# Performance work log

Measured on AMD Instinct MI355X. Metric: run time of the kernel, lower is better.

Reference implementation:

```python
import jax, jax.numpy as jnp
import numpy as np
from jax import lax

B, C, H, W = 4, 128, 256, 256
HEADS = 8
HIDDEN = int(C * 2)  # ffn_expansion_factor=2
THETA = 0.7


def _p(key, shape, scale=0.05):
    return jax.random.normal(key, shape, dtype=jnp.float32) * scale


def setup_inputs() -> dict:
    key = jax.random.key(0)
    ks = jax.random.split(key, 32)
    inp = {
        'ms': jax.random.normal(ks[0], (B, C, H, W), dtype=jnp.float32),
        'pan': jax.random.normal(ks[1], (B, C, H, W), dtype=jnp.float32),
        # LayerNorms (WithBias)
        'ln1_w': jnp.ones((C,), jnp.float32),
        'ln1_b': jnp.zeros((C,), jnp.float32),
        'ln2_w': jnp.ones((2 * C,), jnp.float32),
        'ln2_b': jnp.zeros((2 * C,), jnp.float32),
        # Attention (bias=False)
        'qkv_w': _p(ks[2], (C, C)),            # 1x1 conv weight [out,in]
        'dw_w': _p(ks[3], (C, 1, 3, 3)),       # depthwise 3x3 (Conv2d_cd)
        'temperature': jnp.ones((HEADS, 1, 1), jnp.float32),
        'proj_w': _p(ks[4], (C, C)),
        # Freprocess (default bias=True)
        'pre1_w': _p(ks[5], (C, C)), 'pre1_b': jnp.zeros((C,), jnp.float32),
        'pre2_w': _p(ks[6], (C, C)), 'pre2_b': jnp.zeros((C,), jnp.float32),
        'amp1_w': _p(ks[7], (C, 2 * C)), 'amp1_b': jnp.zeros((C,), jnp.float32),
        'amp2_w': _p(ks[8], (C, C)), 'amp2_b': jnp.zeros((C,), jnp.float32),
        'pha1_w': _p(ks[9], (C, 2 * C)), 'pha1_b': jnp.zeros((C,), jnp.float32),
        'pha2_w': _p(ks[10], (C, C)), 'pha2_b': jnp.zeros((C,), jnp.float32),
        'post_w': _p(ks[11], (C, C)), 'post_b': jnp.zeros((C,), jnp.float32),
        # FFN (bias=False)
        'pin_w': _p(ks[12], (2 * HIDDEN, 2 * C)),
        'pout_w': _p(ks[13], (C, HIDDEN)),
    }
    return inp


def conv1x1(x, w, b=None):
    y = jnp.einsum('bchw,oc->bohw', x, w)
    if b is not None:
        y = y + b[None, :, None, None]
    return y


def layernorm_c(x, w, b):
    # per-pixel LayerNorm over channel dim (torch var unbiased=False, eps=1e-5)
    mu = jnp.mean(x, axis=1, keepdims=True)
    var = jnp.mean((x - mu) ** 2, axis=1, keepdims=True)
    return (x - mu) / jnp.sqrt(var + 1e-5) * w[None, :, None, None] + b[None, :, None, None]


def dwconv_cd(x, w):
    # central-difference depthwise conv: dw3x3(x) - theta * (sum(kernel) * x)
    y = lax.conv_general_dilated(x, w, (1, 1), ((1, 1), (1, 1)),
                                 dimension_numbers=('NCHW', 'OIHW', 'NCHW'),
                                 feature_group_count=x.shape[1])
    ksum = w.sum(axis=(1, 2, 3))  # (C,)
    return y - THETA * x * ksum[None, :, None, None]


def attention(nms, npan, qkv_w, dw_w, temperature, proj_w):
    b, c, h, w = nms.shape
    ch = c // HEADS
    q = dwconv_cd(conv1x1(nms, qkv_w), dw_w)
    kv = dwconv_cd(conv1x1(npan, qkv_w), dw_w)  # k == v in source
    q = q.reshape(b, HEADS, ch, h * w)
    k = kv.reshape(b, HEADS, ch, h * w)
    v = k
    q = q / jnp.maximum(jnp.linalg.norm(q, axis=-1, keepdims=True), 1e-12)
    k = k / jnp.maximum(jnp.linalg.norm(k, axis=-1, keepdims=True), 1e-12)
    attn = jnp.einsum('bhcn,bhdn->bhcd', q, k) * temperature[None]
    attn = jax.nn.softmax(attn, axis=-1)
    out = jnp.einsum('bhcd,bhdn->bhcn', attn, v).reshape(b, c, h, w)
    return conv1x1(out, proj_w)


def freprocess(msf, panf, pre1_w, pre1_b, pre2_w, pre2_b,
               amp1_w, amp1_b, amp2_w, amp2_b,
               pha1_w, pha1_b, pha2_w, pha2_b, post_w, post_b):
    h, w = msf.shape[-2:]
    msF = jnp.fft.rfft2(conv1x1(msf, pre1_w, pre1_b) + 1e-8)
    panF = jnp.fft.rfft2(conv1x1(panf, pre2_w, pre2_b) + 1e-8)
    amp_in = jnp.concatenate([jnp.abs(msF), jnp.abs(panF)], axis=1)
    pha_in = jnp.concatenate([jnp.angle(msF), jnp.angle(panF)], axis=1)
    amp = conv1x1(jax.nn.leaky_relu(conv1x1(amp_in, amp1_w, amp1_b), 0.1), amp2_w, amp2_b)
    pha = conv1x1(jax.nn.leaky_relu(conv1x1(pha_in, pha1_w, pha1_b), 0.1), pha2_w, pha2_b)
    real = amp * jnp.cos(pha) + 1e-8
    imag = amp * jnp.sin(pha) + 1e-8
    out = jax.lax.complex(real, imag) + 1e-8
    out = jnp.abs(jnp.fft.irfft2(out, s=(h, w)))
    return conv1x1(out, post_w, post_b)


def ffn(x, pin_w, pout_w):
    y = conv1x1(x, pin_w)
    x1, x2 = jnp.split(y, 2, axis=1)
    return conv1x1(jax.nn.gelu(x1, approximate=False) * x2, pout_w)


def reference(ms, pan, ln1_w, ln1_b, ln2_w, ln2_b, qkv_w, dw_w, temperature,
              proj_w, pre1_w, pre1_b, pre2_w, pre2_b, amp1_w, amp1_b, amp2_w,
              amp2_b, pha1_w, pha1_b, pha2_w, pha2_b, post_w, post_b,
              pin_w, pout_w):
    x = ms + attention(layernorm_c(ms, ln1_w, ln1_b),
                       layernorm_c(pan, ln1_w, ln1_b),
                       qkv_w, dw_w, temperature, proj_w)
    frefuse = freprocess(ms, pan, pre1_w, pre1_b, pre2_w, pre2_b,
                         amp1_w, amp1_b, amp2_w, amp2_b,
                         pha1_w, pha1_b, pha2_w, pha2_b, post_w, post_b)
    frespa = jnp.concatenate([x, frefuse], axis=1)
    x = x + ffn(layernorm_c(frespa, ln2_w, ln2_b), pin_w, pout_w)
    return x
```

## Files before the change

### kernel.cpp

```cpp
#include <hip/hip_runtime.h>
#include <math.h>

#define B_ 4
#define C_ 128
#define HW_ 65536
#define H__ 256
#define KF_ 129
#define PLANEF_ 33024

typedef __attribute__((ext_vector_type(8))) short short8v;
typedef __attribute__((ext_vector_type(4))) float f32x4;
typedef __attribute__((ext_vector_type(4))) unsigned short ush4;
typedef __attribute__((ext_vector_type(8))) unsigned short ush8;

__device__ __forceinline__ unsigned short f2bf(float f) {
    union { float f; unsigned u; } v; v.f = f;
    return (unsigned short)((v.u + 0x7FFFu + ((v.u >> 16) & 1u)) >> 16);
}
__device__ __forceinline__ float bf2f(unsigned short s) {
    union { unsigned u; float f; } v; v.u = (unsigned)s << 16;
    return v.f;
}
__device__ __forceinline__ unsigned pack2bf(float2 v) {
    return (unsigned)f2bf(v.x) | ((unsigned)f2bf(v.y) << 16);
}
__device__ __forceinline__ float2 upk(unsigned u) {
    return make_float2(bf2f((unsigned short)(u & 0xffff)), bf2f((unsigned short)(u >> 16)));
}
__device__ __forceinline__ float geluf(float x) {
    float z = 0.70710678118654752f * fabsf(x);
    float t = __fdividef(1.f, fmaf(0.3275911f, z, 1.f));
    float p = fmaf(1.061405429f, t, -1.453152027f);
    p = fmaf(p, t, 1.421413741f);
    p = fmaf(p, t, -0.284496736f);
    p = fmaf(p, t, 0.254829592f);
    p = p * t;
    float erfv = 1.f - p * __expf(-z * z);
    float cdf = (x >= 0.f) ? fmaf(0.5f, erfv, 0.5f) : fmaf(-0.5f, erfv, 0.5f);
    return x * cdf;
}
__device__ __forceinline__ float fatan2(float y, float x) {
    float ax = fabsf(x), ay = fabsf(y);
    float mx = fmaxf(ax, ay), mn = fminf(ax, ay);
    float a = __fdividef(mn, fmaxf(mx, 1e-38f));
    float s = a * a;
    float r = fmaf(0.0208351f, s, -0.0851330f);
    r = fmaf(r, s, 0.1801410f);
    r = fmaf(r, s, -0.3302995f);
    r = fmaf(r, s, 0.9998660f);
    r = r * a;
    if (ay > ax) r = 1.57079632679489662f - r;
    if (x < 0.f) r = 3.14159265358979324f - r;
    return copysignf(r, y);
}
template<int W>
__device__ __forceinline__ char* swz_ptr(unsigned short (*xs)[W], int px, int cb) {
    return (char*)xs + px * (W * 2) + (cb ^ (((px >> 2) & 7) << 4));
}

__global__ __launch_bounds__(256) void tobf16_kernel(const float* __restrict__ src,
                                                     unsigned short* __restrict__ dst, int n)
{
    int i = blockIdx.x * 256 + threadIdx.x;
    if (i < n) dst[i] = f2bf(src[i]);
}

__global__ __launch_bounds__(128) void foldln_kernel(const float* __restrict__ W,
                                                     const float* __restrict__ lnw,
                                                     const float* __restrict__ lnb,
                                                     unsigned short* __restrict__ Wb,
                                                     float* __restrict__ wsum, float* __restrict__ bsum,
                                                     int Cc)
{
    int o = blockIdx.x, t = threadIdx.x;
    float sw = 0.f, sb = 0.f;
    for (int c = t; c < Cc; c += 128) {
        float w = W[(size_t)o * Cc + c];
        float fw = w * lnw[c];
        unsigned short us = f2bf(fw);
        Wb[(size_t)o * Cc + c] = us;
        sw += bf2f(us);
        sb += w * lnb[c];
    }
    __shared__ float r1[128], r2[128];
    r1[t] = sw; r2[t] = sb; __syncthreads();
    for (int st = 64; st; st >>= 1) {
        if (t < st) { r1[t] += r1[t + st]; r2[t] += r2[t + st]; }
        __syncthreads();
    }
    if (!t) { wsum[o] = r1[0]; bsum[o] = r2[0]; }
}

__global__ __launch_bounds__(256) void poutperm_kernel(const float* __restrict__ src,
                                                       unsigned short* __restrict__ dst)
{
    int i = blockIdx.x * 256 + threadIdx.x;
    int half = i >> 14, rem = i & 16383, o = rem >> 7, kp = rem & 127;
    int h = (kp >> 5) * 64 + half * 32 + (kp & 31);
    dst[i] = f2bf(src[o * 256 + h]);
}

__global__ void pinc_kernel(const float* __restrict__ bb, const float* __restrict__ ws,
                            float4* __restrict__ pinC)
{
    int i = threadIdx.x;
    if (i < 256) pinC[i] = make_float4(bb[i], ws[i], bb[i + 256], ws[i + 256]);
}

__global__ void ksum_kernel(const float* __restrict__ dw, float* __restrict__ ks)
{
    int c = threadIdx.x;
    if (c < C_) {
        float s = 0.f;
        for (int k = 0; k < 9; ++k) s += dw[c * 9 + k];
        ks[c] = s;
    }
}

__global__ __launch_bounds__(256) void zero2_kernel(float* __restrict__ a, float* __restrict__ b, int n)
{
    int i = blockIdx.x * 256 + threadIdx.x;
    if (i < n) { a[i] = 0.f; b[i] = 0.f; }
}

template<int INBF, int OUTBF, int PRO, bool LNF>
__global__ __launch_bounds__(256, 3) void mconv2(
    const void* __restrict__ Xv, size_t sx,
    const unsigned short* __restrict__ Wb, int wstride,
    const float* __restrict__ bias,
    const float* __restrict__ res, size_t sres,
    void* __restrict__ Yv, size_t sy, int plane, int flags,
    const float* __restrict__ wsum, const float* __restrict__ bsum)
{
    __shared__ unsigned short xs[128][136];
    __shared__ float2 lnred[LNF ? 8 : 1][LNF ? 128 : 1];
    __shared__ float2 lnmi[LNF ? 128 : 1];
    const int t = threadIdx.x;
    const int bz = blockIdx.z;
    const int p0 = blockIdx.x * 128;
    const int lane = t & 63;
    const int wr = t >> 7, wc = (t >> 6) & 1;
    const int lr = lane >> 4, lc = lane & 15;

    if constexpr (INBF == 0) {
        const float* Xb = (const float*)Xv + (size_t)bz * sx;
        const int px4 = t & 31;
        float s0 = 0.f, s1 = 0.f, s2v = 0.f, s3 = 0.f;
        float q0 = 0.f, q1 = 0.f, q2 = 0.f, q3 = 0.f;
#pragma unroll
        for (int g = 0; g < 2; ++g) {
            float4 st[8];
#pragma unroll
            for (int i = 0; i < 8; ++i) {
                int e = t + (g * 8 + i) * 256;
                int c = e >> 5;
                st[i] = *(const float4*)(Xb + (size_t)c * plane + p0 + px4 * 4);
            }
#pragma unroll
            for (int i = 0; i < 8; ++i) {
                int e = t + (g * 8 + i) * 256;
                int c = e >> 5;
                float a0 = st[i].x, a1 = st[i].y, a2 = st[i].z, a3 = st[i].w;
                if constexpr (PRO == 1) {
                    a0 = a0 > 0.f ? a0 : 0.1f * a0;
                    a1 = a1 > 0.f ? a1 : 0.1f * a1;
                    a2 = a2 > 0.f ? a2 : 0.1f * a2;
                    a3 = a3 > 0.f ? a3 : 0.1f * a3;
                }
                if constexpr (LNF) {
                    s0 += a0; q0 += a0 * a0;
                    s1 += a1; q1 += a1 * a1;
                    s2v += a2; q2 += a2 * a2;
                    s3 += a3; q3 += a3 * a3;
                }
                *(unsigned short*)swz_ptr(xs, px4 * 4 + 0, 2 * c) = f2bf(a0);
                *(unsigned short*)swz_ptr(xs, px4 * 4 + 1, 2 * c) = f2bf(a1);
                *(unsigned short*)swz_ptr(xs, px4 * 4 + 2, 2 * c) = f2bf(a2);
                *(unsigned short*)swz_ptr(xs, px4 * 4 + 3, 2 * c) = f2bf(a3);
            }
        }
        if constexpr (LNF) {
            lnred[t >> 5][px4 * 4 + 0] = make_float2(s0, q0);
            lnred[t >> 5][px4 * 4 + 1] = make_float2(s1, q1);
            lnred[t >> 5][px4 * 4 + 2] = make_float2(s2v, q2);
            lnred[t >> 5][px4 * 4 + 3] = make_float2(s3, q3);
        }
    } else {
        const unsigned short* Xb = (const unsigned short*)Xv + (size_t)bz * sx;
        ush8 st[8];
#pragma unroll
        for (int i = 0; i < 8; ++i) {
            int e = t + i * 256;
            int c = e >> 4, px8 = e & 15;
            st[i] = *(const ush8*)(Xb + (size_t)c * plane + p0 + px8 * 8);
        }
#pragma unroll
        for (int i = 0; i < 8; ++i) {
            int e = t + i * 256;
            int c = e >> 4, px8 = e & 15;
#pragma unroll
            for (int j = 0; j < 8; ++j) {
                unsigned short us = (unsigned short)st[i][j];
                if constexpr (PRO == 1) {
                    float f = bf2f(us);
                    f = f > 0.f ? f : 0.1f * f;
                    us = f2bf(f);
                }
                *(unsigned short*)swz_ptr(xs, px8 * 8 + j, 2 * c) = us;
            }
        }
    }
    __syncthreads();
    if constexpr (LNF) {
        if (t < 128) {
            float ss = 0.f, qq = 0.f;
#pragma unroll
            for (int j = 0; j < 8; ++j) { float2 a = lnred[j][t]; ss += a.x; qq += a.y; }
            float m = ss * (1.f / 128.f);
            float inv = rsqrtf(qq * (1.f / 128.f) - m * m + 1e-5f);
            lnmi[t] = make_float2(m, inv);
        }
        __syncthreads();
    }

    f32x4 acc[4][4];
#pragma unroll
    for (int mi = 0; mi < 4; ++mi)
#pragma unroll
        for (int ni = 0; ni < 4; ++ni) acc[mi][ni] = (f32x4){0.f, 0.f, 0.f, 0.f};

#pragma unroll
    for (int kk = 0; kk < 128; kk += 32) {
        short8v bfr[4];
#pragma unroll
        for (int ni = 0; ni < 4; ++ni)
            bfr[ni] = *(const short8v*)swz_ptr(xs, wc * 64 + ni * 16 + lc, 2 * (kk + lr * 8));
#pragma unroll
        for (int mi = 0; mi < 4; ++mi) {
            int row = wr * 64 + mi * 16 + lc;
            short8v afr = *(const short8v*)(Wb + (size_t)row * wstride + kk + lr * 8);
#pragma unroll
            for (int ni = 0; ni < 4; ++ni)
                acc[mi][ni] = __builtin_amdgcn_mfma_f32_16x16x32_bf16(afr, bfr[ni], acc[mi][ni], 0, 0, 0);
        }
    }

    float2 mrow[4];
    if constexpr (LNF) {
#pragma unroll
        for (int ni = 0; ni < 4; ++ni) mrow[ni] = lnmi[wc * 64 + ni * 16 + lc];
    }

#pragma unroll
    for (int mi = 0; mi < 4; ++mi) {
        int ob = wr * 64 + mi * 16 + lr * 4;
#pragma unroll
        for (int r = 0; r < 4; ++r) {
            int o = ob + r;
            float bv = 0.f, wso = 0.f;
            if constexpr (LNF) { bv = bsum[o]; wso = wsum[o]; }
            else { if (bias) bv = bias[o]; if (flags & 1) bv += 1e-8f; }
#pragma unroll
            for (int ni = 0; ni < 4; ++ni) {
                int px = wc * 64 + ni * 16 + lc;
                float v;
                if constexpr (LNF) {
                    float m = mrow[ni].x, inv = mrow[ni].y;
                    v = acc[mi][ni][r] * inv + bv - m * inv * wso;
                } else {
                    v = acc[mi][ni][r] + bv;
                }
                if constexpr (OUTBF == 0) {
                    float* Y = (float*)Yv;
                    size_t yi = (size_t)bz * sy + (size_t)o * plane + p0 + px;
                    if (res) v += res[(size_t)bz * sres + (size_t)o * plane + p0 + px];
                    Y[yi] = v;
                } else {
                    unsigned short* Y = (unsigned short*)Yv;
                    Y[(size_t)bz * sy + (size_t)o * plane + p0 + px] = f2bf(v);
                }
            }
        }
    }
}

__global__ __launch_bounds__(256, 2) void apconv2(
    const unsigned* __restrict__ T1, const unsigned* __restrict__ T2, size_t sT,
    const unsigned short* __restrict__ Wa1, const unsigned short* __restrict__ Wp1,
    const unsigned short* __restrict__ Wa2, const unsigned short* __restrict__ Wp2,
    const float* __restrict__ ba1, const float* __restrict__ bp1,
    const float* __restrict__ ba2, const float* __restrict__ bp2,
    unsigned short* __restrict__ AMP, unsigned short* __restrict__ PHA, size_t sO)
{
    __shared__ __align__(16) unsigned short buf[2][128][72];
    const int t = threadIdx.x;
    const int bz = blockIdx.z;
    const int p0 = blockIdx.x * 128;
    const int lane = t & 63;
    const int wr = t >> 7, wc = (t >> 6) & 1;
    const int lr = lane >> 4, lc = lane & 15;
    const int px2 = t & 63;

    typedef unsigned short (*row72)[72];
    typedef unsigned short (*row144)[144];
    row72 xa = (row72)buf[0];
    row72 xp = (row72)buf[1];
    row144 hb = (row144)&buf[0][0][0];

    f32x4 aa[4][4], ap[4][4];
#pragma unroll
    for (int mi = 0; mi < 4; ++mi)
#pragma unroll
        for (int ni = 0; ni < 4; ++ni) { aa[mi][ni] = (f32x4){0.f,0.f,0.f,0.f}; ap[mi][ni] = (f32x4){0.f,0.f,0.f,0.f}; }

    for (int ch = 0; ch < 256; ch += 64) {
        const unsigned* Ts = ((ch < 128) ? T1 : T2) + (size_t)bz * sT + (size_t)(ch & 127) * PLANEF_;
#pragma unroll
        for (int g = 0; g < 2; ++g) {
            uint2 st[8];
#pragma unroll
            for (int i = 0; i < 8; ++i) {
                int e = t + (g * 8 + i) * 256;
                int c = e >> 6;
                st[i] = *(const uint2*)(Ts + (size_t)c * PLANEF_ + p0 + px2 * 2);
            }
#pragma unroll
            for (int i = 0; i < 8; ++i) {
                int e = t + (g * 8 + i) * 256;
                int c = e >> 6;
                float2 z0 = upk(st[i].x), z1 = upk(st[i].y);
                float m0 = sqrtf(z0.x * z0.x + z0.y * z0.y);
                float m1 = sqrtf(z1.x * z1.x + z1.y * z1.y);
                float a0 = fatan2(z0.y, z0.x);
                float a1 = fatan2(z1.y, z1.x);
                *(unsigned short*)swz_ptr(xa, px2 * 2 + 0, 2 * c) = f2bf(m0);
                *(unsigned short*)swz_ptr(xa, px2 * 2 + 1, 2 * c) = f2bf(m1);
                *(unsigned short*)swz_ptr(xp, px2 * 2 + 0, 2 * c) = f2bf(a0);
                *(unsigned short*)swz_ptr(xp, px2 * 2 + 1, 2 * c) = f2bf(a1);
            }
        }
        __syncthreads();
#pragma unroll
        for (int kk = 0; kk < 64; kk += 32) {
            short8v bfa[4], bfp[4];
#pragma unroll
            for (int ni = 0; ni < 4; ++ni) {
                bfa[ni] = *(const short8v*)swz_ptr(xa, wc * 64 + ni * 16 + lc, 2 * (kk + lr * 8));
                bfp[ni] = *(const short8v*)swz_ptr(xp, wc * 64 + ni * 16 + lc, 2 * (kk + lr * 8));
            }
#pragma unroll
            for (int mi = 0; mi < 4; ++mi) {
                int row = wr * 64 + mi * 16 + lc;
                short8v afa = *(const short8v*)(Wa1 + (size_t)row * 256 + ch + kk + lr * 8);
                short8v afp = *(const short8v*)(Wp1 + (size_t)row * 256 + ch + kk + lr * 8);
#pragma unroll
                for (int ni = 0; ni < 4; ++ni) {
                    aa[mi][ni] = __builtin_amdgcn_mfma_f32_16x16x32_bf16(afa, bfa[ni], aa[mi][ni], 0, 0, 0);
                    ap[mi][ni] = __builtin_amdgcn_mfma_f32_16x16x32_bf16(afp, bfp[ni], ap[mi][ni], 0, 0, 0);
                }
            }
        }
        __syncthreads();
    }

#pragma unroll
    for (int mi = 0; mi < 4; ++mi)
#pragma unroll
        for (int r = 0; r < 4; ++r) {
            int o = wr * 64 + mi * 16 + lr * 4 + r;
            float bva = ba1[o];
#pragma unroll
            for (int ni = 0; ni < 4; ++ni) {
                int px = wc * 64 + ni * 16 + lc;
                float v = aa[mi][ni][r] + bva;
                v = v > 0.f ? v : 0.1f * v;
                *(unsigned short*)swz_ptr(hb, px, 2 * o) = f2bf(v);
            }
        }
    __syncthreads();
    {
        f32x4 acc[4][4];
#pragma unroll
        for (int mi = 0; mi < 4; ++mi)
#pragma unroll
            for (int ni = 0; ni < 4; ++ni) acc[mi][ni] = (f32x4){0.f,0.f,0.f,0.f};
#pragma unroll
        for (int kk = 0; kk < 128; kk += 32) {
            short8v bfr[4];
#pragma unroll
            for (int ni = 0; ni < 4; ++ni)
                bfr[ni] = *(const short8v*)swz_ptr(hb, wc * 64 + ni * 16 + lc, 2 * (kk + lr * 8));
#pragma unroll
            for (int mi = 0; mi < 4; ++mi) {
                int row = wr * 64 + mi * 16 + lc;
                short8v afr = *(const short8v*)(Wa2 + (size_t)row * 128 + kk + lr * 8);
#pragma unroll
                for (int ni = 0; ni < 4; ++ni)
                    acc[mi][ni] = __builtin_amdgcn_mfma_f32_16x16x32_bf16(afr, bfr[ni], acc[mi][ni], 0, 0, 0);
            }
        }
#pragma unroll
        for (int mi = 0; mi < 4; ++mi)
#pragma unroll
            for (int r = 0; r < 4; ++r) {
                int o = wr * 64 + mi * 16 + lr * 4 + r;
                float bv = ba2[o];
#pragma unroll
                for (int ni = 0; ni < 4; ++ni) {
                    int px = wc * 64 + ni * 16 + lc;
                    AMP[(size_t)bz * sO + (size_t)o * PLANEF_ + p0 + px] = f2bf(acc[mi][ni][r] + bv);
                }
            }
    }
    __syncthreads();

#pragma unroll
    for (int mi = 0; mi < 4; ++mi)
#pragma unroll
        for (int r = 0; r < 4; ++r) {
            int o = wr * 64 + mi * 16 + lr * 4 + r;
            float bvp = bp1[o];
#pragma unroll
            for (int ni = 0; ni < 4; ++ni) {
                int px = wc * 64 + ni * 16 + lc;
                float v = ap[mi][ni][r] + bvp;
                v = v > 0.f ? v : 0.1f * v;
                *(unsigned short*)swz_ptr(hb, px, 2 * o) = f2bf(v);
            }
        }
    __syncthreads();
    {
        f32x4 acc[4][4];
#pragma unroll
        for (int mi = 0; mi < 4; ++mi)
#pragma unroll
            for (int ni = 0; ni < 4; ++ni) acc[mi][ni] = (f32x4){0.f,0.f,0.f,0.f};
#pragma unroll
        for (int kk = 0; kk < 128; kk += 32) {
            short8v bfr[4];
#pragma unroll
            for (int ni = 0; ni < 4; ++ni)
                bfr[ni] = *(const short8v*)swz_ptr(hb, wc * 64 + ni * 16 + lc, 2 * (kk + lr * 8));
#pragma unroll
            for (int mi = 0; mi < 4; ++mi) {
                int row = wr * 64 + mi * 16 + lc;
                short8v afr = *(const short8v*)(Wp2 + (size_t)row * 128 + kk + lr * 8);
#pragma unroll
                for (int ni = 0; ni < 4; ++ni)
                    acc[mi][ni] = __builtin_amdgcn_mfma_f32_16x16x32_bf16(afr, bfr[ni], acc[mi][ni], 0, 0, 0);
            }
        }
#pragma unroll
        for (int mi = 0; mi < 4; ++mi)
#pragma unroll
            for (int r = 0; r < 4; ++r) {
                int o = wr * 64 + mi * 16 + lr * 4 + r;
                float bv = bp2[o];
#pragma unroll
                for (int ni = 0; ni < 4; ++ni) {
                    int px = wc * 64 + ni * 16 + lc;
                    PHA[(size_t)bz * sO + (size_t)o * PLANEF_ + p0 + px] = f2bf(acc[mi][ni][r] + bv);
                }
            }
    }
}

__global__ __launch_bounds__(256, 3) void ffn_mfma5(
    const float* __restrict__ x, const unsigned short* __restrict__ fre,
    const unsigned short* __restrict__ pinb,
    const unsigned short* __restrict__ pout2,
    const float4* __restrict__ pinC,
    float* __restrict__ out)
{
    __shared__ unsigned short xs[64][264];
    __shared__ unsigned short hs[64][136];
    __shared__ float2 muinv[64];
    float2* sred = (float2*)&hs[0][0];
    const int b = blockIdx.y;
    const size_t p0 = (size_t)blockIdx.x * 64;
    const int t = threadIdx.x;
    const int wave = t >> 6, lane = t & 63;
    const int lr = lane >> 4, lc = lane & 15;
    const int px4 = t & 15;

    float s0 = 0.f, s1 = 0.f, s2v = 0.f, s3 = 0.f;
    float q0 = 0.f, q1 = 0.f, q2 = 0.f, q3 = 0.f;
    {
        float4 stx[8];
        ush4 stf[8];
#pragma unroll
        for (int i = 0; i < 8; ++i) {
            int e = t + i * 256;
            int c = e >> 4;
            stx[i] = *(const float4*)(x + ((size_t)b * 128 + c) * HW_ + p0 + px4 * 4);
        }
#pragma unroll
        for (int i = 0; i < 8; ++i) {
            int e = t + i * 256;
            int c = e >> 4;
            stf[i] = *(const ush4*)(fre + (size_t)b * 8388608 + (size_t)c * HW_ + p0 + px4 * 4);
        }
#pragma unroll
        for (int i = 0; i < 8; ++i) {
            int e = t + i * 256;
            int c = e >> 4;
            float a0 = stx[i].x, a1 = stx[i].y, a2 = stx[i].z, a3 = stx[i].w;
            s0 += a0; q0 += a0 * a0;
            s1 += a1; q1 += a1 * a1;
            s2v += a2; q2 += a2 * a2;
            s3 += a3; q3 += a3 * a3;
            *(unsigned short*)swz_ptr(xs, px4 * 4 + 0, 2 * c) = f2bf(a0);
            *(unsigned short*)swz_ptr(xs, px4 * 4 + 1, 2 * c) = f2bf(a1);
            *(unsigned short*)swz_ptr(xs, px4 * 4 + 2, 2 * c) = f2bf(a2);
            *(unsigned short*)swz_ptr(xs, px4 * 4 + 3, 2 * c) = f2bf(a3);
        }
#pragma unroll
        for (int i = 0; i < 8; ++i) {
            int e = t + i * 256;
            int c = e >> 4;
            float a0 = bf2f((unsigned short)stf[i][0]);
            float a1 = bf2f((unsigned short)stf[i][1]);
            float a2 = bf2f((unsigned short)stf[i][2]);
            float a3 = bf2f((unsigned short)stf[i][3]);
            s0 += a0; q0 += a0 * a0;
            s1 += a1; q1 += a1 * a1;
            s2v += a2; q2 += a2 * a2;
            s3 += a3; q3 += a3 * a3;
            *(unsigned short*)swz_ptr(xs, px4 * 4 + 0, 2 * (128 + c)) = (unsigned short)stf[i][0];
            *(unsigned short*)swz_ptr(xs, px4 * 4 + 1, 2 * (128 + c)) = (unsigned short)stf[i][1];
            *(unsigned short*)swz_ptr(xs, px4 * 4 + 2, 2 * (128 + c)) = (unsigned short)stf[i][2];
            *(unsigned short*)swz_ptr(xs, px4 * 4 + 3, 2 * (128 + c)) = (unsigned short)stf[i][3];
        }
    }
    sred[(t >> 4) * 64 + px4 * 4 + 0] = make_float2(s0, q0);
    sred[(t >> 4) * 64 + px4 * 4 + 1] = make_float2(s1, q1);
    sred[(t >> 4) * 64 + px4 * 4 + 2] = make_float2(s2v, q2);
    sred[(t >> 4) * 64 + px4 * 4 + 3] = make_float2(s3, q3);
    __syncthreads();
    if (t < 64) {
        float ss = 0.f, qq = 0.f;
#pragma unroll
        for (int j = 0; j < 16; ++j) { float2 a = sred[j * 64 + t]; ss += a.x; qq += a.y; }
        float m = ss * (1.f / 256.f);
        float inv = rsqrtf(qq * (1.f / 256.f) - m * m + 1e-5f);
        muinv[t] = make_float2(m, inv);
    }
    __syncthreads();

    float2 mrow[4];
#pragma unroll
    for (int ni = 0; ni < 4; ++ni) mrow[ni] = muinv[ni * 16 + lc];

    f32x4 oc[2][4];
#pragma unroll
    for (int mi = 0; mi < 2; ++mi)
#pragma unroll
        for (int ni = 0; ni < 4; ++ni) oc[mi][ni] = (f32x4){0.f, 0.f, 0.f, 0.f};

#pragma unroll
    for (int half = 0; half < 2; ++half) {
        f32x4 a1[2][4], a2[2][4];
#pragma unroll
        for (int mi = 0; mi < 2; ++mi)
#pragma unroll
            for (int ni = 0; ni < 4; ++ni) { a1[mi][ni] = (f32x4){0.f,0.f,0.f,0.f}; a2[mi][ni] = (f32x4){0.f,0.f,0.f,0.f}; }

#pragma unroll
        for (int k0 = 0; k0 < 256; k0 += 32) {
            short8v bfr[4];
#pragma unroll
            for (int ni = 0; ni < 4; ++ni)
                bfr[ni] = *(const short8v*)swz_ptr(xs, ni * 16 + lc, 2 * (k0 + lr * 8));
#pragma unroll
            for (int mi = 0; mi < 2; ++mi) {
                int hrow = wave * 64 + half * 32 + mi * 16 + lc;
                short8v af1 = *(const short8v*)(pinb + (size_t)hrow * 256 + k0 + lr * 8);
                short8v af2 = *(const short8v*)(pinb + (size_t)(hrow + 256) * 256 + k0 + lr * 8);
#pragma unroll
                for (int ni = 0; ni < 4; ++ni) {
                    a1[mi][ni] = __builtin_amdgcn_mfma_f32_16x16x32_bf16(af1, bfr[ni], a1[mi][ni], 0, 0, 0);
                    a2[mi][ni] = __builtin_amdgcn_mfma_f32_16x16x32_bf16(af2, bfr[ni], a2[mi][ni], 0, 0, 0);
                }
            }
        }
        __syncthreads();
#pragma unroll
        for (int mi = 0; mi < 2; ++mi)
#pragma unroll
            for (int r = 0; r < 4; ++r) {
                int ho = wave * 64 + half * 32 + mi * 16 + lr * 4 + r;
                float4 bwc = pinC[ho];
                int kp = wave * 32 + mi * 16 + lr * 4 + r;
#pragma unroll
                for (int ni = 0; ni < 4; ++ni) {
                    float m = mrow[ni].x, inv = mrow[ni].y;
                    float v1 = a1[mi][ni][r] * inv + bwc.x - m * inv * bwc.y;
                    float v2 = a2[mi][ni][r] * inv + bwc.z - m * inv * bwc.w;
                    hs[ni * 16 + lc][kp] = f2bf(geluf(v1) * v2);
                }
            }
        __syncthreads();
#pragma unroll
        for (int k0 = 0; k0 < 128; k0 += 32) {
            short8v bfr2[4];
#pragma unroll
            for (int ni = 0; ni < 4; ++ni)
                bfr2[ni] = *(const short8v*)&hs[ni * 16 + lc][k0 + lr * 8];
#pragma unroll
            for (int mi = 0; mi < 2; ++mi) {
                int orow = wave * 32 + mi * 16 + lc;
                short8v af = *(const short8v*)(pout2 + half * 16384 + orow * 128 + k0 + lr * 8);
#pragma unroll
                for (int ni = 0; ni < 4; ++ni)
                    oc[mi][ni] = __builtin_amdgcn_mfma_f32_16x16x32_bf16(af, bfr2[ni], oc[mi][ni], 0, 0, 0);
            }
        }
    }

#pragma unroll
    for (int mi = 0; mi < 2; ++mi)
#pragma unroll
        for (int r = 0; r < 4; ++r) {
            int o = wave * 32 + mi * 16 + lr * 4 + r;
#pragma unroll
            for (int ni = 0; ni < 4; ++ni) {
                size_t yi = ((size_t)b * 128 + o) * HW_ + p0 + ni * 16 + lc;
                out[yi] = oc[mi][ni][r] + x[yi];
            }
        }
}

__global__ __launch_bounds__(256) void dwconv2(const unsigned short* __restrict__ X, size_t sx,
                                               const float* __restrict__ w9,
                                               const float* __restrict__ ksum,
                                               unsigned short* __restrict__ Y, size_t sy,
                                               float* __restrict__ ssq)
{
    int bz = blockIdx.z;
    int c = blockIdx.y;
    int p4 = blockIdx.x * 256 + threadIdx.x;
    int p0 = p4 * 4;
    int i = p0 >> 8, j0 = p0 & 255;
    const unsigned short* xp = X + (size_t)bz * sx + (size_t)c * HW_;
    const float* wc = w9 + c * 9;
    float a[4] = {0.f, 0.f, 0.f, 0.f};
    float ctr[4];
#pragma unroll
    for (int di = -1; di <= 1; ++di) {
        int ii = i + di;
        if (ii < 0 || ii > 255) continue;
        const unsigned short* row = xp + ii * 256;
        ush4 m4 = *(const ush4*)(row + j0);
        float lft = (j0 > 0) ? bf2f(row[j0 - 1]) : 0.f;
        float rgt = (j0 < 252) ? bf2f(row[j0 + 4]) : 0.f;
        float v[6] = {lft, bf2f((unsigned short)m4[0]), bf2f((unsigned short)m4[1]),
                      bf2f((unsigned short)m4[2]), bf2f((unsigned short)m4[3]), rgt};
        if (di == 0) { ctr[0] = v[1]; ctr[1] = v[2]; ctr[2] = v[3]; ctr[3] = v[4]; }
        float w0 = wc[(di + 1) * 3], w1 = wc[(di + 1) * 3 + 1], w2 = wc[(di + 1) * 3 + 2];
#pragma unroll
        for (int k = 0; k < 4; ++k) a[k] += w0 * v[k] + w1 * v[k + 1] + w2 * v[k + 2];
    }
    float km = 0.7f * ksum[c];
    float o0 = a[0] - km * ctr[0], o1 = a[1] - km * ctr[1];
    float o2 = a[2] - km * ctr[2], o3 = a[3] - km * ctr[3];
    ush4 ov;
    ov[0] = f2bf(o0); ov[1] = f2bf(o1); ov[2] = f2bf(o2); ov[3] = f2bf(o3);
    *(ush4*)(Y + (size_t)bz * sy + (size_t)c * HW_ + p0) = ov;

    float q = o0 * o0 + o1 * o1 + o2 * o2 + o3 * o3;
    __shared__ float red[256];
    red[threadIdx.x] = q; __syncthreads();
    for (int st = 128; st; st >>= 1) {
        if (threadIdx.x < st) red[threadIdx.x] += red[threadIdx.x + st];
        __syncthreads();
    }
    if (!threadIdx.x) atomicAdd(&ssq[bz * C_ + c], red[0]);
}

__global__ __launch_bounds__(256) void gram_kernel(const unsigned short* __restrict__ Q, size_t sq,
                                                   const unsigned short* __restrict__ K, size_t sk,
                                                   float* __restrict__ part)
{
    int sl = blockIdx.x, h = blockIdx.y, bz = blockIdx.z;
    const unsigned short* qb = Q + (size_t)bz * sq + (size_t)(h * 16) * HW_;
    const unsigned short* kb = K + (size_t)bz * sk + (size_t)(h * 16) * HW_;
    __shared__ __align__(16) float qs[16][68];
    __shared__ __align__(16) float ks[16][68];
    int c = threadIdx.x >> 4, d = threadIdx.x & 15;
    float acc = 0.f;
    for (int n0 = sl * 2048; n0 < (sl + 1) * 2048; n0 += 64) {
        {
            int cc = threadIdx.x >> 4, nn4 = threadIdx.x & 15;
            ush4 qv = *(const ush4*)(qb + (size_t)cc * HW_ + n0 + nn4 * 4);
            ush4 kv = *(const ush4*)(kb + (size_t)cc * HW_ + n0 + nn4 * 4);
#pragma unroll
            for (int j = 0; j < 4; ++j) {
                qs[cc][nn4 * 4 + j] = bf2f((unsigned short)qv[j]);
                ks[cc][nn4 * 4 + j] = bf2f((unsigned short)kv[j]);
            }
        }
        __syncthreads();
#pragma unroll
        for (int nn = 0; nn < 64; nn += 4) {
            float4 qv = *(const float4*)&qs[c][nn];
            float4 kv = *(const float4*)&ks[d][nn];
            acc += qv.x * kv.x + qv.y * kv.y + qv.z * kv.z + qv.w * kv.w;
        }
        __syncthreads();
    }
    part[((size_t)(bz * 8 + h) * 32 + sl) * 256 + threadIdx.x] = acc;
}

__global__ __launch_bounds__(256) void softmax_kernel(const float* __restrict__ part,
                                                      const float* __restrict__ nqsq,
                                                      const float* __restrict__ nksq,
                                                      const float* __restrict__ temp,
                                                      float* __restrict__ attn)
{
    int h = blockIdx.x, bz = blockIdx.y;
    int t = threadIdx.x;
    int c = t >> 4, d = t & 15;
    float g = 0.f;
    for (int sl = 0; sl < 32; ++sl) g += part[((size_t)(bz * 8 + h) * 32 + sl) * 256 + t];
    float nqv = fmaxf(sqrtf(nqsq[bz * C_ + h * 16 + c]), 1e-12f);
    float nkv = fmaxf(sqrtf(nksq[bz * C_ + h * 16 + d]), 1e-12f);
    g *= temp[h] / (nqv * nkv);
    float m = g;
#pragma unroll
    for (int off = 8; off; off >>= 1) m = fmaxf(m, __shfl_xor(m, off, 16));
    float e = __expf(g - m);
    float ssum = e;
#pragma unroll
    for (int off = 8; off; off >>= 1) ssum += __shfl_xor(ssum, off, 16);
    attn[(bz * 8 + h) * 256 + t] = e / ssum;
}

__global__ __launch_bounds__(256) void av_kernel(const float* __restrict__ attn,
                                                 const unsigned short* __restrict__ V, size_t sv,
                                                 unsigned short* __restrict__ Y, size_t sy)
{
    __shared__ __align__(16) float kv[16][260];
    __shared__ __align__(16) float at[16][16];
    int tile = blockIdx.x, h = blockIdx.y, bz = blockIdx.z;
    int n0 = tile * 256, t = threadIdx.x;
    const unsigned short* vb = V + (size_t)bz * sv + (size_t)(h * 16) * HW_;
    at[t >> 4][t & 15] = attn[(size_t)(bz * 8 + h) * 256 + (t & 15) * 16 + (t >> 4)];
#pragma unroll
    for (int i = 0; i < 4; ++i) {
        int e = t + i * 256;
        int d = e >> 6, nn4 = e & 63;
        ush4 v4 = *(const ush4*)(vb + (size_t)d * HW_ + n0 + nn4 * 4);
#pragma unroll
        for (int j = 0; j < 4; ++j) kv[d][nn4 * 4 + j] = bf2f((unsigned short)v4[j]);
    }
    __syncthreads();
    float acc[16];
#pragma unroll
    for (int cc = 0; cc < 16; ++cc) acc[cc] = 0.f;
#pragma unroll
    for (int d = 0; d < 16; ++d) {
        float kvv = kv[d][t];
        float4 a0 = *(const float4*)&at[d][0];
        float4 a1 = *(const float4*)&at[d][4];
        float4 a2 = *(const float4*)&at[d][8];
        float4 a3 = *(const float4*)&at[d][12];
        acc[0]  += a0.x * kvv; acc[1]  += a0.y * kvv; acc[2]  += a0.z * kvv; acc[3]  += a0.w * kvv;
        acc[4]  += a1.x * kvv; acc[5]  += a1.y * kvv; acc[6]  += a1.z * kvv; acc[7]  += a1.w * kvv;
        acc[8]  += a2.x * kvv; acc[9]  += a2.y * kvv; acc[10] += a2.z * kvv; acc[11] += a2.w * kvv;
        acc[12] += a3.x * kvv; acc[13] += a3.y * kvv; acc[14] += a3.z * kvv; acc[15] += a3.w * kvv;
    }
    unsigned short* yb = Y + (size_t)bz * sy + (size_t)(h * 16) * HW_ + n0 + t;
#pragma unroll
    for (int cc = 0; cc < 16; ++cc) yb[(size_t)cc * HW_] = f2bf(acc[cc]);
}

__device__ __forceinline__ void fft_stages(float2* row, const float2* tw, int lane)
{
#pragma unroll
    for (int s = 1; s <= 8; ++s) {
        const int half = 1 << (s - 1);
#pragma unroll
        for (int r = 0; r < 4; ++r) {
            int jb = lane + r * 32;
            int j = jb & (half - 1);
            int g = jb >> (s - 1);
            int i1 = (g << s) + j;
            float2 w = tw[j << (8 - s)];
            float2 u = row[i1];
            float2 q = row[i1 + half];
            float2 v = make_float2(q.x * w.x - q.y * w.y, q.x * w.y + q.y * w.x);
            row[i1]        = make_float2(u.x + v.x, u.y + v.y);
            row[i1 + half] = make_float2(u.x - v.x, u.y - v.y);
        }
        __builtin_amdgcn_wave_barrier();
    }
    __syncthreads();
}

#define PI2_ 6.28318530717958647692f

__global__ __launch_bounds__(256) void rfft_rowsT(const unsigned short* __restrict__ X, size_t sx,
                                                  unsigned* __restrict__ T, size_t st)
{
    __shared__ float2 sd[8][256];
    __shared__ float2 tw[128];
    int t = threadIdx.x;
    int bz = blockIdx.y;
    if (t < 128) { float sn, cs; __sincosf(-PI2_ * (float)t * (1.f / 256.f), &sn, &cs); tw[t] = make_float2(cs, sn); }
    size_t r0 = (size_t)blockIdx.x * 8;
    int c = (int)(r0 >> 8), h0 = (int)(r0 & 255);
    const unsigned short* Xb = X + (size_t)bz * sx;
#pragma unroll
    for (int ii = 0; ii < 2; ++ii) {
        int e = t + ii * 256;
        int j = e >> 6, i4 = e & 63;
        ush4 v4 = *(const ush4*)(Xb + (r0 + j) * 256 + i4 * 4);
#pragma unroll
        for (int k2 = 0; k2 < 4; ++k2)
            sd[j][__brev((unsigned)(i4 * 4 + k2)) >> 24] = make_float2(bf2f((unsigned short)v4[k2]), 0.f);
    }
    __syncthreads();
    fft_stages(sd[t >> 5], tw, t & 31);
    unsigned* base = T + (size_t)bz * st + (size_t)c * PLANEF_;
    for (int e = t; e < 8 * 129; e += 256) {
        int j = e & 7, k = e >> 3;
        base[(size_t)k * 256 + h0 + j] = pack2bf(sd[j][k]);
    }
}

__global__ __launch_bounds__(256) void cfftT_fwd(unsigned* __restrict__ T, size_t st)
{
    __shared__ float2 sd[8][256];
    __shared__ float2 tw[128];
    int t = threadIdx.x;
    int bz = blockIdx.z;
    if (t < 128) { float sn, cs; __sincosf(-PI2_ * (float)t * (1.f / 256.f), &sn, &cs); tw[t] = make_float2(cs, sn); }
    int k0 = blockIdx.x * 8;
    int c = blockIdx.y;
    unsigned* base = T + (size_t)bz * st + (size_t)c * PLANEF_;
    for (int e = t; e < 2048; e += 256) {
        int j = e >> 8, i = e & 255;
        int k = k0 + j;
        float2 v = (k < KF_) ? upk(base[(size_t)k * 256 + i]) : make_float2(0.f, 0.f);
        sd[j][__brev((unsigned)i) >> 24] = v;
    }
    __syncthreads();
    fft_stages(sd[t >> 5], tw, t & 31);
    for (int e = t; e < 2048; e += 256) {
        int j = e >> 8, i = e & 255;
        int k = k0 + j;
        if (k < KF_) base[(size_t)k * 256 + i] = pack2bf(sd[j][i]);
    }
}

__global__ __launch_bounds__(256) void cifft_combine(const unsigned short* __restrict__ amp, size_t sa,
                                                     const unsigned short* __restrict__ pha, size_t sp,
                                                     unsigned* __restrict__ S, size_t ss)
{
    __shared__ float2 sd[8][256];
    __shared__ float2 tw[128];
    int t = threadIdx.x;
    int bz = blockIdx.z;
    if (t < 128) { float sn, cs; __sincosf(PI2_ * (float)t * (1.f / 256.f), &sn, &cs); tw[t] = make_float2(cs, sn); }
    int k0 = blockIdx.x * 8;
    int c = blockIdx.y;
    const unsigned short* ab = amp + (size_t)bz * sa + (size_t)c * PLANEF_;
    const unsigned short* pb = pha + (size_t)bz * sp + (size_t)c * PLANEF_;
    for (int e = t; e < 2048; e += 256) {
        int j = e >> 8, i = e & 255;
        int k = k0 + j;
        float2 v = make_float2(0.f, 0.f);
        if (k < KF_) {
            float a = bf2f(ab[(size_t)k * 256 + i]);
            float p = bf2f(pb[(size_t)k * 256 + i]);
            float sn, cs;
            __sincosf(p, &sn, &cs);
            v = make_float2(a * cs + 2e-8f, a * sn + 1e-8f);
        }
        sd[j][__brev((unsigned)i) >> 24] = v;
    }
    __syncthreads();
    fft_stages(sd[t >> 5], tw, t & 31);
    unsigned* base = S + (size_t)bz * ss + (size_t)c * PLANEF_;
    for (int e = t; e < 2048; e += 256) {
        int j = e & 7, h = e >> 3;
        int k = k0 + j;
        if (k < KF_) {
            float2 o = sd[j][h];
            base[(size_t)h * KF_ + k] = pack2bf(make_float2(o.x * (1.f / 256.f), o.y * (1.f / 256.f)));
        }
    }
}

__global__ __launch_bounds__(256) void irfft_rows8_abs(const unsigned* __restrict__ S, size_t ss,
                                                       unsigned short* __restrict__ Y, size_t sy)
{
    __shared__ float2 sd[8][256];
    __shared__ float2 tw[128];
    int t = threadIdx.x;
    int bz = blockIdx.y;
    if (t < 128) { float sn, cs; __sincosf(PI2_ * (float)t * (1.f / 256.f), &sn, &cs); tw[t] = make_float2(cs, sn); }
    size_t r0 = (size_t)blockIdx.x * 8;
    const unsigned* Sb = S + (size_t)bz * ss;
    for (int e = t; e < 2048; e += 256) {
        int j = e >> 8, i = e & 255;
        const unsigned* row = Sb + (r0 + j) * 129;
        float2 v;
        if (i < 129) v = upk(row[i]);
        else { float2 w2 = upk(row[256 - i]); v = make_float2(w2.x, -w2.y); }
        sd[j][__brev((unsigned)i) >> 24] = v;
    }
    __syncthreads();
    fft_stages(sd[t >> 5], tw, t & 31);
    unsigned short* Yb = Y + (size_t)bz * sy;
    for (int e = t; e < 2048; e += 256) {
        int j = e >> 8, i = e & 255;
        Yb[(r0 + j) * 256 + i] = f2bf(fabsf(sd[j][i].x * (1.f / 256.f)));
    }
}

extern "C" void kernel_launch(void* const* d_in, const int* in_sizes, int n_in,
                              void* d_out, int out_size, void* d_ws, size_t ws_size,
                              hipStream_t stream)
{
    (void)in_sizes; (void)n_in; (void)out_size;
    const float* ms    = (const float*)d_in[0];
    const float* pan   = (const float*)d_in[1];
    const float* ln1w  = (const float*)d_in[2];
    const float* ln1b  = (const float*)d_in[3];
    const float* ln2w  = (const float*)d_in[4];
    const float* ln2b  = (const float*)d_in[5];
    const float* qkvw  = (const float*)d_in[6];
    const float* dww   = (const float*)d_in[7];
    const float* temp  = (const float*)d_in[8];
    const float* projw = (const float*)d_in[9];
    const float* pre1w = (const float*)d_in[10];
    const float* pre1b = (const float*)d_in[11];
    const float* pre2w = (const float*)d_in[12];
    const float* pre2b = (const float*)d_in[13];
    const float* amp1w = (const float*)d_in[14];
    const float* amp1b = (const float*)d_in[15];
    const float* amp2w = (const float*)d_in[16];
    const float* amp2b = (const float*)d_in[17];
    const float* pha1w = (const float*)d_in[18];
    const float* pha1b = (const float*)d_in[19];
    const float* pha2w = (const float*)d_in[20];
    const float* pha2b = (const float*)d_in[21];
    const float* postw = (const float*)d_in[22];
    const float* postb = (const float*)d_in[23];
    const float* pinw  = (const float*)d_in[24];
    const float* poutw = (const float*)d_in[25];

    const size_t SLOT  = 8454144;
    const size_t CHWu  = 8388608;
    const size_t CPFu  = 4227072;
    const size_t SPECu = 4227072;
    const size_t PARAMU = 344064;
    const size_t PARAMF = 273792;

    auto needB = [&](int nb) -> size_t {
        return 2ull * (33554432ull + (size_t)nb * 3ull * SLOT + PARAMU) + 4ull * PARAMF + 64;
    };
    int NB = (ws_size >= needB(4)) ? 4 : ((ws_size >= needB(2)) ? 2 : 1);

    unsigned short* F  = (unsigned short*)d_ws;
    unsigned short* U0 = F + 33554432;
    unsigned short* U1 = U0 + (size_t)NB * SLOT;
    unsigned short* U2 = U1 + (size_t)NB * SLOT;
    unsigned short* w_qkv   = U2 + (size_t)NB * SLOT;
    unsigned short* w_proj  = w_qkv  + 16384;
    unsigned short* w_pre1  = w_proj + 16384;
    unsigned short* w_pre2  = w_pre1 + 16384;
    unsigned short* w_post  = w_pre2 + 16384;
    unsigned short* w_amp1  = w_post + 16384;
    unsigned short* w_pha1  = w_amp1 + 32768;
    unsigned short* w_amp2  = w_pha1 + 32768;
    unsigned short* w_pha2  = w_amp2 + 16384;
    unsigned short* w_pin   = w_pha2 + 16384;
    unsigned short* w_pout2 = w_pin  + 131072;
    float* fpar   = (float*)(w_pout2 + 32768);
    float* ksumP  = fpar;
    float* nqsq   = ksumP + 128;
    float* nksq   = nqsq  + 512;
    float* attnP  = nksq  + 512;
    float* partP  = attnP + 8192;
    float* qkv_ws = partP + 262144;
    float* qkv_bb = qkv_ws + 128;
    float* pin_ws = qkv_bb + 128;
    float* pin_bb = pin_ws + 512;
    float* pinC   = pin_bb + 512;

    float* xout = (float*)d_out;

    auto CVT = [&](const float* src, unsigned short* dst, int n) {
        tobf16_kernel<<<(n + 255) / 256, 256, 0, stream>>>(src, dst, n);
    };
    foldln_kernel<<<128, 128, 0, stream>>>(qkvw, ln1w, ln1b, w_qkv, qkv_ws, qkv_bb, 128);
    foldln_kernel<<<512, 128, 0, stream>>>(pinw, ln2w, ln2b, w_pin, pin_ws, pin_bb, 256);
    CVT(projw, w_proj, 16384);
    CVT(pre1w, w_pre1, 16384); CVT(pre2w, w_pre2, 16384);
    CVT(postw, w_post, 16384);
    CVT(amp1w, w_amp1, 32768); CVT(pha1w, w_pha1, 32768);
    CVT(amp2w, w_amp2, 16384); CVT(pha2w, w_pha2, 16384);
    poutperm_kernel<<<128, 256, 0, stream>>>(poutw, w_pout2);
    pinc_kernel<<<1, 256, 0, stream>>>(pin_bb, pin_ws, (float4*)pinC);
    ksum_kernel<<<1, 128, 0, stream>>>(dww, ksumP);

    const size_t CHW = (size_t)C_ * HW_;
    const float* NUL = nullptr;

    for (int b0 = 0; b0 < B_; b0 += NB) {
        const float* msb  = ms  + (size_t)b0 * CHW;
        const float* panb = pan + (size_t)b0 * CHW;
        float* xb = xout + (size_t)b0 * CHW;
        unsigned short* freb = F + (size_t)b0 * CHWu;
        dim3 gz(512, 1, NB);
        dim3 gzf(258, 1, NB);

        zero2_kernel<<<(NB * 128 + 255) / 256, 256, 0, stream>>>(nqsq, nksq, NB * 128);
        mconv2<0, 1, 0, true><<<gz, 256, 0, stream>>>(
            msb, CHW, w_qkv, 128, nullptr, nullptr, 0, U0, SLOT, HW_, 0, qkv_ws, qkv_bb);
        dwconv2<<<dim3(64, 128, NB), 256, 0, stream>>>(U0, SLOT, dww, ksumP, U1, SLOT, nqsq);
        mconv2<0, 1, 0, true><<<gz, 256, 0, stream>>>(
            panb, CHW, w_qkv, 128, nullptr, nullptr, 0, U0, SLOT, HW_, 0, qkv_ws, qkv_bb);
        dwconv2<<<dim3(64, 128, NB), 256, 0, stream>>>(U0, SLOT, dww, ksumP, U2, SLOT, nksq);
        gram_kernel<<<dim3(32, 8, NB), 256, 0, stream>>>(U1, SLOT, U2, SLOT, partP);
        softmax_kernel<<<dim3(8, NB), 256, 0, stream>>>(partP, nqsq, nksq, temp, attnP);
        av_kernel<<<dim3(256, 8, NB), 256, 0, stream>>>(attnP, U2, SLOT, U0, SLOT);
        mconv2<1, 0, 0, false><<<gz, 256, 0, stream>>>(
            U0, SLOT, w_proj, 128, nullptr, msb, CHW, xb, CHW, HW_, 0, NUL, NUL);

        mconv2<0, 1, 0, false><<<gz, 256, 0, stream>>>(
            msb, CHW, w_pre1, 128, pre1b, nullptr, 0, U0, SLOT, HW_, 1, NUL, NUL);
        rfft_rowsT<<<dim3(4096, NB), 256, 0, stream>>>(U0, SLOT, (unsigned*)(void*)U1, SPECu);
        cfftT_fwd<<<dim3(17, 128, NB), 256, 0, stream>>>((unsigned*)(void*)U1, SPECu);
        mconv2<0, 1, 0, false><<<gz, 256, 0, stream>>>(
            panb, CHW, w_pre2, 128, pre2b, nullptr, 0, U0, SLOT, HW_, 1, NUL, NUL);
        rfft_rowsT<<<dim3(4096, NB), 256, 0, stream>>>(U0, SLOT, (unsigned*)(void*)U2, SPECu);
        cfftT_fwd<<<dim3(17, 128, NB), 256, 0, stream>>>((unsigned*)(void*)U2, SPECu);
        apconv2<<<gzf, 256, 0, stream>>>(
            (const unsigned*)(void*)U1, (const unsigned*)(void*)U2, SPECu,
            w_amp1, w_pha1, w_amp2, w_pha2, amp1b, pha1b, amp2b, pha2b,
            U0, U0 + CPFu, SLOT);
        cifft_combine<<<dim3(17, 128, NB), 256, 0, stream>>>(
            U0, SLOT, U0 + CPFu, SLOT, (unsigned*)(void*)U2, SPECu);
        irfft_rows8_abs<<<dim3(4096, NB), 256, 0, stream>>>((unsigned*)(void*)U2, SPECu, U0, SLOT);
        mconv2<1, 1, 0, false><<<gz, 256, 0, stream>>>(
            U0, SLOT, w_post, 128, postb, nullptr, 0, freb, CHWu, HW_, 0, NUL, NUL);
    }

    ffn_mfma5<<<dim3(HW_ / 64, B_), 256, 0, stream>>>(xout, F, w_pin, w_pout2, (const float4*)pinC, xout);
}
```

Measured before the change: 1.798 ms.

## Fuse row and column FFT passes into single per-plane LDS-resident 2D FFT kernels

Replaces the separate row-FFT and column-FFT kernels, each a global round trip of the spectrum, with one block per (channel, batch) plane. The block keeps the whole 129x257 bf16-complex plane in shared memory (about 132 KB) and runs both passes there. The inverse path likewise fuses the amp/phase combine, column IFFT and row IRFFT with abs, and mconv2 launch bounds are raised from 3 to 4 waves. The cost is only 512 blocks per FFT kernel at one block per CU, with long serial loops per block, so latency hiding is much lower.

```diff
diff --git a/kernel.cpp b/kernel.cpp
--- a/kernel.cpp
+++ b/kernel.cpp
@@ -7,6 +7,7 @@
 #define H__ 256
 #define KF_ 129
 #define PLANEF_ 33024
+#define PLD_ 257
 
 typedef __attribute__((ext_vector_type(8))) short short8v;
 typedef __attribute__((ext_vector_type(4))) float f32x4;
@@ -124,7 +125,7 @@
 }
 
 template<int INBF, int OUTBF, int PRO, bool LNF>
-__global__ __launch_bounds__(256, 3) void mconv2(
+__global__ __launch_bounds__(256, 4) void mconv2(
     const void* __restrict__ Xv, size_t sx,
     const unsigned short* __restrict__ Wb, int wstride,
     const float* __restrict__ bias,
@@ -799,123 +800,126 @@
 
 #define PI2_ 6.28318530717958647692f
 
-__global__ __launch_bounds__(256) void rfft_rowsT(const unsigned short* __restrict__ X, size_t sx,
-                                                  unsigned* __restrict__ T, size_t st)
-{
+__global__ __launch_bounds__(256, 1) void fft2d_fwd(
+    const unsigned short* __restrict__ X, size_t sx,
+    unsigned* __restrict__ T, size_t st)
+{
+    __shared__ unsigned plane[129 * PLD_];
     __shared__ float2 sd[8][256];
     __shared__ float2 tw[128];
-    int t = threadIdx.x;
-    int bz = blockIdx.y;
+    const int t = threadIdx.x;
+    const int c = blockIdx.x, bz = blockIdx.y;
     if (t < 128) { float sn, cs; __sincosf(-PI2_ * (float)t * (1.f / 256.f), &sn, &cs); tw[t] = make_float2(cs, sn); }
-    size_t r0 = (size_t)blockIdx.x * 8;
-    int c = (int)(r0 >> 8), h0 = (int)(r0 & 255);
-    const unsigned short* Xb = X + (size_t)bz * sx;
-#pragma unroll
-    for (int ii = 0; ii < 2; ++ii) {
-        int e = t + ii * 256;
-        int j = e >> 6, i4 = e & 63;
-        ush4 v4 = *(const ush4*)(Xb + (r0 + j) * 256 + i4 * 4);
-#pragma unroll
-        for (int k2 = 0; k2 < 4; ++k2)
-            sd[j][__brev((unsigned)(i4 * 4 + k2)) >> 24] = make_float2(bf2f((unsigned short)v4[k2]), 0.f);
+    const unsigned short* Xc = X + (size_t)bz * sx + (size_t)c * HW_;
+    const int j = t >> 5;
+    const int i0 = (t & 31) * 8;
+
+    ush8 pref = *(const ush8*)(Xc + (size_t)t * 8);
+    for (int rg = 0; rg < 32; ++rg) {
+        ush8 cur = pref;
+        if (rg < 31) pref = *(const ush8*)(Xc + (size_t)(rg + 1) * 2048 + (size_t)t * 8);
+        __syncthreads();
+#pragma unroll
+        for (int k2 = 0; k2 < 8; ++k2)
+            sd[j][__brev((unsigned)(i0 + k2)) >> 24] = make_float2(bf2f((unsigned short)cur[k2]), 0.f);
+        __syncthreads();
+        fft_stages(sd[j], tw, t & 31);
+        for (int e = t; e < 129 * 8; e += 256) {
+            int j2 = e & 7, k = e >> 3;
+            plane[k * PLD_ + rg * 8 + j2] = pack2bf(sd[j2][k]);
+        }
     }
     __syncthreads();
-    fft_stages(sd[t >> 5], tw, t & 31);
-    unsigned* base = T + (size_t)bz * st + (size_t)c * PLANEF_;
-    for (int e = t; e < 8 * 129; e += 256) {
-        int j = e & 7, k = e >> 3;
-        base[(size_t)k * 256 + h0 + j] = pack2bf(sd[j][k]);
-    }
-}
-
-__global__ __launch_bounds__(256) void cfftT_fwd(unsigned* __restrict__ T, size_t st)
-{
+
+    for (int kg = 0; kg < 17; ++kg) {
+        for (int e = t; e < 2048; e += 256) {
+            int j2 = e >> 8, i = e & 255;
+            int k = kg * 8 + j2;
+            float2 v = (k < KF_) ? upk(plane[k * PLD_ + i]) : make_float2(0.f, 0.f);
+            sd[j2][__brev((unsigned)i) >> 24] = v;
+        }
+        __syncthreads();
+        fft_stages(sd[j], tw, t & 31);
+        for (int e = t; e < 2048; e += 256) {
+            int j2 = e >> 8, i = e & 255;
+            int k = kg * 8 + j2;
+            if (k < KF_) plane[k * PLD_ + i] = pack2bf(sd[j2][i]);
+        }
+        __syncthreads();
+    }
+
+    unsigned* Tc = T + (size_t)bz * st + (size_t)c * PLANEF_;
+    for (int e = t; e < 129 * 256; e += 256) {
+        int k = e >> 8, h = e & 255;
+        Tc[e] = plane[k * PLD_ + h];
+    }
+}
+
+__global__ __launch_bounds__(256, 1) void fft2d_inv_abs(
+    const unsigned short* __restrict__ amp, const unsigned short* __restrict__ pha, size_t sa,
+    unsigned short* __restrict__ Y, size_t sy)
+{
+    __shared__ unsigned plane[129 * PLD_];
     __shared__ float2 sd[8][256];
     __shared__ float2 tw[128];
-    int t = threadIdx.x;
-    int bz = blockIdx.z;
-    if (t < 128) { float sn, cs; __sincosf(-PI2_ * (float)t * (1.f / 256.f), &sn, &cs); tw[t] = make_float2(cs, sn); }
-    int k0 = blockIdx.x * 8;
-    int c = blockIdx.y;
-    unsigned* base = T + (size_t)bz * st + (size_t)c * PLANEF_;
-    for (int e = t; e < 2048; e += 256) {
-        int j = e >> 8, i = e & 255;
-        int k = k0 + j;
-        float2 v = (k < KF_) ? upk(base[(size_t)k * 256 + i]) : make_float2(0.f, 0.f);
-        sd[j][__brev((unsigned)i) >> 24] = v;
-    }
-    __syncthreads();
-    fft_stages(sd[t >> 5], tw, t & 31);
-    for (int e = t; e < 2048; e += 256) {
-        int j = e >> 8, i = e & 255;
-        int k = k0 + j;
-        if (k < KF_) base[(size_t)k * 256 + i] = pack2bf(sd[j][i]);
-    }
-}
-
-__global__ __launch_bounds__(256) void cifft_combine(const unsigned short* __restrict__ amp, size_t sa,
-                                                     const unsigned short* __restrict__ pha, size_t sp,
-                                                     unsigned* __restrict__ S, size_t ss)
-{
-    __shared__ float2 sd[8][256];
-    __shared__ float2 tw[128];
-    int t = threadIdx.x;
-    int bz = blockIdx.z;
+    const int t = threadIdx.x;
+    const int c = blockIdx.x, bz = blockIdx.y;
     if (t < 128) { float sn, cs; __sincosf(PI2_ * (float)t * (1.f / 256.f), &sn, &cs); tw[t] = make_float2(cs, sn); }
-    int k0 = blockIdx.x * 8;
-    int c = blockIdx.y;
-    const unsigned short* ab = amp + (size_t)bz * sa + (size_t)c * PLANEF_;
-    const unsigned short* pb = pha + (size_t)bz * sp + (size_t)c * PLANEF_;
-    for (int e = t; e < 2048; e += 256) {
-        int j = e >> 8, i = e & 255;
-        int k = k0 + j;
-        float2 v = make_float2(0.f, 0.f);
-        if (k < KF_) {
-            float a = bf2f(ab[(size_t)k * 256 + i]);
-            float p = bf2f(pb[(size_t)k * 256 + i]);
-            float sn, cs;
-            __sincosf(p, &sn, &cs);
-            v = make_float2(a * cs + 2e-8f, a * sn + 1e-8f);
-        }
-        sd[j][__brev((unsigned)i) >> 24] = v;
-    }
-    __syncthreads();
-    fft_stages(sd[t >> 5], tw, t & 31);
-    unsigned* base = S + (size_t)bz * ss + (size_t)c * PLANEF_;
-    for (int e = t; e < 2048; e += 256) {
-        int j = e & 7, h = e >> 3;
-        int k = k0 + j;
-        if (k < KF_) {
-            float2 o = sd[j][h];
-            base[(size_t)h * KF_ + k] = pack2bf(make_float2(o.x * (1.f / 256.f), o.y * (1.f / 256.f)));
-        }
-    }
-}
-
-__global__ __launch_bounds__(256) void irfft_rows8_abs(const unsigned* __restrict__ S, size_t ss,
-                                                       unsigned short* __restrict__ Y, size_t sy)
-{
-    __shared__ float2 sd[8][256];
-    __shared__ float2 tw[128];
-    int t = threadIdx.x;
-    int bz = blockIdx.y;
-    if (t < 128) { float sn, cs; __sincosf(PI2_ * (float)t * (1.f / 256.f), &sn, &cs); tw[t] = make_float2(cs, sn); }
-    size_t r0 = (size_t)blockIdx.x * 8;
-    const unsigned* Sb = S + (size_t)bz * ss;
-    for (int e = t; e < 2048; e += 256) {
-        int j = e >> 8, i = e & 255;
-        const unsigned* row = Sb + (r0 + j) * 129;
-        float2 v;
-        if (i < 129) v = upk(row[i]);
-        else { float2 w2 = upk(row[256 - i]); v = make_float2(w2.x, -w2.y); }
-        sd[j][__brev((unsigned)i) >> 24] = v;
-    }
-    __syncthreads();
-    fft_stages(sd[t >> 5], tw, t & 31);
-    unsigned short* Yb = Y + (size_t)bz * sy;
-    for (int e = t; e < 2048; e += 256) {
-        int j = e >> 8, i = e & 255;
-        Yb[(r0 + j) * 256 + i] = f2bf(fabsf(sd[j][i].x * (1.f / 256.f)));
+    const unsigned short* ac = amp + (size_t)bz * sa + (size_t)c * PLANEF_;
+    const unsigned short* pc = pha + (size_t)bz * sa + (size_t)c * PLANEF_;
+    const int j = t >> 5;
+
+    for (int kg = 0; kg < 17; ++kg) {
+        for (int e = t; e < 512; e += 256) {
+            int j2 = e >> 6, i4 = e & 63;
+            int k = kg * 8 + j2;
+            float2 v[4] = {{0.f,0.f},{0.f,0.f},{0.f,0.f},{0.f,0.f}};
+            if (k < KF_) {
+                ush4 a4 = *(const ush4*)(ac + (size_t)k * 256 + i4 * 4);
+                ush4 p4 = *(const ush4*)(pc + (size_t)k * 256 + i4 * 4);
+#pragma unroll
+                for (int q = 0; q < 4; ++q) {
+                    float a = bf2f((unsigned short)a4[q]);
+                    float p = bf2f((unsigned short)p4[q]);
+                    float sn, cs;
+                    __sincosf(p, &sn, &cs);
+                    v[q] = make_float2(a * cs + 2e-8f, a * sn + 1e-8f);
+                }
+            }
+#pragma unroll
+            for (int q = 0; q < 4; ++q)
+                sd[j2][__brev((unsigned)(i4 * 4 + q)) >> 24] = v[q];
+        }
+        __syncthreads();
+        fft_stages(sd[j], tw, t & 31);
+        for (int e = t; e < 2048; e += 256) {
+            int j2 = e >> 8, i = e & 255;
+            int k = kg * 8 + j2;
+            if (k < KF_) {
+                float2 o = sd[j2][i];
+                plane[k * PLD_ + i] = pack2bf(make_float2(o.x * (1.f / 256.f), o.y * (1.f / 256.f)));
+            }
+        }
+        __syncthreads();
+    }
+
+    unsigned short* Yc = Y + (size_t)bz * sy + (size_t)c * HW_;
+    for (int hg = 0; hg < 32; ++hg) {
+        for (int e = t; e < 2048; e += 256) {
+            int j2 = e >> 8, i = e & 255;
+            int h = hg * 8 + j2;
+            float2 v;
+            if (i < KF_) v = upk(plane[i * PLD_ + h]);
+            else { float2 w2 = upk(plane[(256 - i) * PLD_ + h]); v = make_float2(w2.x, -w2.y); }
+            sd[j2][__brev((unsigned)i) >> 24] = v;
+        }
+        __syncthreads();
+        fft_stages(sd[j], tw, t & 31);
+        for (int e = t; e < 2048; e += 256) {
+            int j2 = e >> 8, i = e & 255;
+            Yc[(size_t)(hg * 8 + j2) * 256 + i] = f2bf(fabsf(sd[j2][i].x * (1.f / 256.f)));
+        }
+        __syncthreads();
     }
 }
 
@@ -1032,21 +1036,17 @@
 
         mconv2<0, 1, 0, false><<<gz, 256, 0, stream>>>(
             msb, CHW, w_pre1, 128, pre1b, nullptr, 0, U0, SLOT, HW_, 1, NUL, NUL);
-        rfft_rowsT<<<dim3(4096, NB), 256, 0, stream>>>(U0, SLOT, (unsigned*)(void*)U1, SPECu);
-        cfftT_fwd<<<dim3(17, 128, NB), 256, 0, stream>>>((unsigned*)(void*)U1, SPECu);
+        fft2d_fwd<<<dim3(128, NB), 256, 0, stream>>>(U0, SLOT, (unsigned*)(void*)U1, SPECu);
         mconv2<0, 1, 0, false><<<gz, 256, 0, stream>>>(
             panb, CHW, w_pre2, 128, pre2b, nullptr, 0, U0, SLOT, HW_, 1, NUL, NUL);
-        rfft_rowsT<<<dim3(4096, NB), 256, 0, stream>>>(U0, SLOT, (unsigned*)(void*)U2, SPECu);
-        cfftT_fwd<<<dim3(17, 128, NB), 256, 0, stream>>>((unsigned*)(void*)U2, SPECu);
+        fft2d_fwd<<<dim3(128, NB), 256, 0, stream>>>(U0, SLOT, (unsigned*)(void*)U2, SPECu);
         apconv2<<<gzf, 256, 0, stream>>>(
             (const unsigned*)(void*)U1, (const unsigned*)(void*)U2, SPECu,
             w_amp1, w_pha1, w_amp2, w_pha2, amp1b, pha1b, amp2b, pha2b,
             U0, U0 + CPFu, SLOT);
-        cifft_combine<<<dim3(17, 128, NB), 256, 0, stream>>>(
-            U0, SLOT, U0 + CPFu, SLOT, (unsigned*)(void*)U2, SPECu);
-        irfft_rows8_abs<<<dim3(4096, NB), 256, 0, stream>>>((unsigned*)(void*)U2, SPECu, U0, SLOT);
+        fft2d_inv_abs<<<dim3(128, NB), 256, 0, stream>>>(U0, U0 + CPFu, SLOT, U2, SLOT);
         mconv2<1, 1, 0, false><<<gz, 256, 0, stream>>>(
-            U0, SLOT, w_post, 128, postb, nullptr, 0, freb, CHWu, HW_, 0, NUL, NUL);
+            U2, SLOT, w_post, 128, postb, nullptr, 0, freb, CHWu, HW_, 0, NUL, NUL);
     }
 
     ffn_mfma5<<<dim3(HW_ / 64, B_), 256, 0, stream>>>(xout, F, w_pin, w_pout2, (const float4*)pinC, xout);
```

After: 2.033 ms. +13.1%, slower.
